# Kernel tuning notes

Measured on AMD Instinct MI355X. Metric: run time of the kernel, lower is better.

## Reference

```python
import jax, jax.numpy as jnp
import numpy as np

GN_GROUPS = 32
GN_EPS = 1e-5


def conv1x1(x, w, b):
    # x: [B,C,H,W], w: [O,C], b: [O]
    return jnp.einsum('bchw,oc->bohw', x, w) + b[None, :, None, None]


def maxpool2(x):
    B, C, H, W = x.shape
    return x.reshape(B, C, H // 2, 2, W // 2, 2).max(axis=(3, 5))


def group_norm(x, w, b, groups=GN_GROUPS, eps=GN_EPS):
    B, C, H, W = x.shape
    xg = x.reshape(B, groups, -1)
    m = xg.mean(axis=-1, keepdims=True)
    v = xg.var(axis=-1, keepdims=True)
    xn = ((xg - m) * jax.lax.rsqrt(v + eps)).reshape(B, C, H, W)
    return xn * w[None, :, None, None] + b[None, :, None, None]


def setup_inputs() -> dict:
    key = jax.random.key(0)
    ks = jax.random.split(key, 8)
    B, C, Ci, H, W = 4, 128, 64, 96, 96
    s_in = 1.0 / np.sqrt(C)
    s_ic = 1.0 / np.sqrt(Ci)
    return {
        'x': jax.random.normal(ks[0], (B, C, H, W), jnp.float32),
        'w_theta': jax.random.normal(ks[1], (Ci, C), jnp.float32) * s_in,
        'b_theta': jnp.zeros((Ci,), jnp.float32),
        'w_phi': jax.random.normal(ks[2], (Ci, C), jnp.float32) * s_in,
        'b_phi': jnp.zeros((Ci,), jnp.float32),
        'w_g': jax.random.normal(ks[3], (Ci, C), jnp.float32) * s_in,
        'b_g': jnp.zeros((Ci,), jnp.float32),
        'w_W': jax.random.normal(ks[4], (C, Ci), jnp.float32) * s_ic,
        'b_W': jnp.zeros((C,), jnp.float32),
        'gn_w': jnp.ones((C,), jnp.float32),
        'gn_b': jnp.zeros((C,), jnp.float32),
    }


def reference(x, w_theta, b_theta, w_phi, b_phi, w_g, b_g, w_W, b_W, gn_w, gn_b):
    B, C, H, W = x.shape
    Ci = w_theta.shape[0]
    # projections (1x1 convs); phi and g are 2x2 max-pooled (sub_sample=True)
    theta = conv1x1(x, w_theta, b_theta).reshape(B, Ci, H * W)          # [B,Ci,N]
    phi = maxpool2(conv1x1(x, w_phi, b_phi)).reshape(B, Ci, -1)         # [B,Ci,N']
    g = maxpool2(conv1x1(x, w_g, b_g)).reshape(B, Ci, -1)               # [B,Ci,N']
    # unscaled single-head attention
    f = jnp.einsum('bcn,bcm->bnm', theta, phi)                          # [B,N,N']
    f = jax.nn.softmax(f, axis=-1)
    y = jnp.einsum('bnm,bcm->bcn', f, g).reshape(B, Ci, H, W)           # [B,Ci,H,W]
    w_y = group_norm(conv1x1(y, w_W, b_W), gn_w, gn_b)
    return w_y + x
```

## Files before the change

### kernel.cpp

```cpp
#include <hip/hip_runtime.h>
#include <math.h>

#define B_ 4
#define C_ 128
#define CI_ 64
#define H_ 96
#define W_ 96
#define HW_ (H_*W_)
#define NP_ 2304
#define GROUPS_ 32
#define EPS_ 1e-5f
#define KVT_ 32
#define NT_ (NP_/KVT_)
#define NBLK_ 288

typedef _Float16 f16x8 __attribute__((ext_vector_type(8)));
typedef _Float16 f16x2 __attribute__((ext_vector_type(2)));
typedef __attribute__((ext_vector_type(4))) float f32x4;

__device__ inline f32x4 mfma16h(f16x8 a, f16x8 b, f32x4 c) {
    return __builtin_amdgcn_mfma_f32_16x16x32_f16(a, b, c, 0, 0, 0);
}
__device__ inline float h2f(unsigned short s) {
    return (float)__builtin_bit_cast(_Float16, s);
}
__device__ inline unsigned pk_f16(float a, float b) {
    return __builtin_bit_cast(unsigned, __builtin_amdgcn_cvt_pkrtz(a, b));
}
__device__ inline f16x8 pk8(float v0, float v1, float v2, float v3,
                            float v4, float v5, float v6, float v7) {
    uint4 u = { pk_f16(v0, v1), pk_f16(v2, v3), pk_f16(v4, v5), pk_f16(v6, v7) };
    return __builtin_bit_cast(f16x8, u);
}
__device__ inline void gload_lds16(const void* g, void* l) {
    __builtin_amdgcn_global_load_lds(
        (const __attribute__((address_space(1))) void*)reinterpret_cast<uintptr_t>(g),
        (__attribute__((address_space(3))) void*)(unsigned)reinterpret_cast<uintptr_t>(l),
        16, 0, 0);
}

__global__ __launch_bounds__(256) void wprep_kernel(
    const float* __restrict__ w_theta, const float* __restrict__ w_phi,
    const float* __restrict__ w_g,     const float* __restrict__ w_W,
    unsigned short* __restrict__ Whall)
{
    const int idx = blockIdx.x * 256 + threadIdx.x;
    float v;
    if      (idx <  8192) v = w_theta[idx];
    else if (idx < 16384) v = w_phi[idx - 8192];
    else if (idx < 24576) v = w_g[idx - 16384];
    else                  v = w_W[idx - 24576];
    Whall[idx] = __builtin_bit_cast(unsigned short, (_Float16)v);
}

__global__ __launch_bounds__(128) void proj_kernel(
    const float* __restrict__ x, const unsigned short* __restrict__ Whall,
    const float* __restrict__ b_theta, const float* __restrict__ b_phi,
    const float* __restrict__ b_g,
    unsigned short* __restrict__ Qo, unsigned short* __restrict__ phiF,
    unsigned short* __restrict__ gF)
{
    __shared__ __align__(16) unsigned short pb[2][16 * 72];

    const int t    = threadIdx.x;
    const int wv   = t >> 6;
    const int lane = t & 63;
    const int lr   = lane & 15;
    const int lg   = lane >> 4;
    const int b    = blockIdx.y;
    const int px0  = blockIdx.x * 32 + wv * 16;

    const float* xb = x + (size_t)b * C_ * HW_ + px0 + lr;
    f16x8 xa[4];
    #pragma unroll
    for (int u = 0; u < 4; ++u) {
        const float* p = xb + (size_t)(u * 32 + lg * 8) * HW_;
        xa[u] = pk8(p[0], p[(size_t)HW_], p[2 * (size_t)HW_], p[3 * (size_t)HW_],
                    p[4 * (size_t)HW_], p[5 * (size_t)HW_], p[6 * (size_t)HW_],
                    p[7 * (size_t)HW_]);
    }

    #pragma unroll
    for (int mat = 0; mat < 3; ++mat) {
        const unsigned short* Whp = Whall + mat * 8192;
        const float* bsel = (mat == 0) ? b_theta : (mat == 1) ? b_phi : b_g;
        unsigned short* osel = (mat == 0) ? Qo : (mat == 1) ? phiF : gF;

        f32x4 D[4];
        #pragma unroll
        for (int ct = 0; ct < 4; ++ct) D[ct] = (f32x4){0.f, 0.f, 0.f, 0.f};
        #pragma unroll
        for (int u = 0; u < 4; ++u)
            #pragma unroll
            for (int ct = 0; ct < 4; ++ct) {
                f16x8 wb = *(const f16x8*)&Whp[(ct * 16 + lr) * 128 + u * 32 + lg * 8];
                D[ct] = mfma16h(xa[u], wb, D[ct]);
            }

        #pragma unroll
        for (int ct = 0; ct < 4; ++ct) {
            const float bi = bsel[ct * 16 + lr];
            #pragma unroll
            for (int r2 = 0; r2 < 4; ++r2)
                pb[wv][(4 * lg + r2) * 72 + ct * 16 + lr] =
                    __builtin_bit_cast(unsigned short, (_Float16)(D[ct][r2] + bi));
        }
        {
            const int px = lane >> 2, ch = lane & 3;
            f16x8 y0 = *(const f16x8*)&pb[wv][px * 72 + ch * 16];
            f16x8 y1 = *(const f16x8*)&pb[wv][px * 72 + ch * 16 + 8];
            unsigned short* op = osel + ((size_t)b * HW_ + px0 + px) * CI_ + ch * 16;
            *(f16x8*)op       = y0;
            *(f16x8*)(op + 8) = y1;
        }
    }
}

__global__ __launch_bounds__(256) void pool_kernel(
    const unsigned short* __restrict__ phiF, const unsigned short* __restrict__ gF,
    unsigned short* __restrict__ Ko, unsigned short* __restrict__ Vt)
{
    __shared__ unsigned short vbuf[32][66];
    const int t  = threadIdx.x;
    const int b  = blockIdx.y;
    const int m0 = blockIdx.x * 32;

    {
        const int ci = t & 63;
        #pragma unroll
        for (int i = 0; i < 8; ++i) {
            const int ml = (t >> 6) + 4 * i;
            const int m  = m0 + ml;
            const int ph = m / 48, pw = m % 48;
            const size_t base = ((size_t)b * HW_ + (ph * 2) * W_ + pw * 2) * CI_ + ci;
            const unsigned short* pk_ = phiF + base;
            const unsigned short* pg_ = gF + base;
            float kv = fmaxf(fmaxf(h2f(pk_[0]), h2f(pk_[CI_])),
                             fmaxf(h2f(pk_[(size_t)W_ * CI_]), h2f(pk_[(size_t)(W_ + 1) * CI_])));
            float gv = fmaxf(fmaxf(h2f(pg_[0]), h2f(pg_[CI_])),
                             fmaxf(h2f(pg_[(size_t)W_ * CI_]), h2f(pg_[(size_t)(W_ + 1) * CI_])));
            Ko[((size_t)b * NP_ + m) * CI_ + ci] =
                __builtin_bit_cast(unsigned short, (_Float16)kv);
            vbuf[ml][ci] = __builtin_bit_cast(unsigned short, (_Float16)gv);
        }
    }
    __syncthreads();
    {
        const int ml = t & 31;
        const int ms = (8 * ((ml >> 2) & 3) + 4 * ((ml >> 4) & 1) + (ml & 3));
        #pragma unroll
        for (int i = 0; i < 8; ++i) {
            const int ci = (t >> 5) + 8 * i;
            Vt[((size_t)b * CI_ + ci) * NP_ + m0 + ms] = vbuf[ml][ci];
        }
    }
}

__global__ __launch_bounds__(128) void attn_kernel(
    const unsigned short* __restrict__ Qg, const unsigned short* __restrict__ Kg,
    const unsigned short* __restrict__ Vt, unsigned short* __restrict__ Yh)
{
    __shared__ unsigned char Klds[2][4096];
    __shared__ unsigned char Vlds[2][4096];

    const int t    = threadIdx.x;
    const int wv   = t >> 6;
    const int lane = t & 63;
    const int lr   = lane & 15;
    const int lg   = lane >> 4;
    const int b    = blockIdx.y;
    const int q0   = blockIdx.x * 32 + wv * 16;

    const int krow = lane >> 3;
    const int kchk = (lane & 7) ^ krow;
    const int vrow = lane >> 2;
    const int vchk = (lane & 3) ^ (vrow & 3);

    const unsigned short* Kb = Kg + (size_t)b * NP_ * CI_;
    const unsigned short* Vb = Vt + (size_t)b * CI_ * NP_;

    f16x8 qf[2];
    #pragma unroll
    for (int u = 0; u < 2; ++u)
        qf[u] = *(const f16x8*)(Qg + ((size_t)b * HW_ + q0 + lr) * CI_ + u * 32 + lg * 8);

    f32x4 o_acc[4];
    #pragma unroll
    for (int dt = 0; dt < 4; ++dt) o_acc[dt] = (f32x4){0.f, 0.f, 0.f, 0.f};
    float mrun = -1e30f, lrun = 0.f;

#define STAGE(BUF, TT)                                                          \
    {                                                                           \
        const int kv0_ = (TT) * KVT_;                                           \
        if (wv == 0) {                                                          \
            _Pragma("unroll")                                                   \
            for (int i = 0; i < 4; ++i)                                         \
                gload_lds16(Kb + (size_t)(kv0_ + 8 * i + krow) * CI_ + kchk * 8,\
                            &Klds[BUF][i * 1024]);                              \
        } else {                                                                \
            _Pragma("unroll")                                                   \
            for (int i = 0; i < 4; ++i)                                         \
                gload_lds16(Vb + (size_t)(16 * i + vrow) * NP_ + kv0_ + vchk * 8,\
                            &Vlds[BUF][i * 1024]);                              \
        }                                                                       \
    }

#define COMPUTE(BUF)                                                            \
    {                                                                           \
        f16x8 kf[2][2];                                                         \
        _Pragma("unroll")                                                       \
        for (int u = 0; u < 2; ++u)                                             \
            _Pragma("unroll")                                                   \
            for (int k4 = 0; k4 < 2; ++k4)                                      \
                kf[u][k4] = *(const f16x8*)&Klds[BUF][(k4 * 16 + lr) * 128      \
                                + (((4 * u + lg) ^ (lr & 7)) << 4)];            \
        f32x4 s[2];                                                             \
        s[0] = (f32x4){0.f, 0.f, 0.f, 0.f};                                     \
        s[1] = (f32x4){0.f, 0.f, 0.f, 0.f};                                     \
        __builtin_amdgcn_s_setprio(1);                                          \
        _Pragma("unroll")                                                       \
        for (int u = 0; u < 2; ++u) {                                           \
            s[0] = mfma16h(kf[u][0], qf[u], s[0]);                              \
            s[1] = mfma16h(kf[u][1], qf[u], s[1]);                              \
        }                                                                       \
        __builtin_amdgcn_s_setprio(0);                                          \
        float tmax = fmaxf(fmaxf(fmaxf(s[0][0], s[0][1]),                       \
                                 fmaxf(s[0][2], s[0][3])),                      \
                           fmaxf(fmaxf(s[1][0], s[1][1]),                       \
                                 fmaxf(s[1][2], s[1][3])));                     \
        if (!__all(tmax <= mrun + 8.0f)) {                                      \
            tmax = fmaxf(tmax, __shfl_xor(tmax, 16));                           \
            tmax = fmaxf(tmax, __shfl_xor(tmax, 32));                           \
            const float mnew = fmaxf(mrun, tmax);                               \
            const float sc = __expf(mrun - mnew);                               \
            lrun *= sc;                                                         \
            _Pragma("unroll")                                                   \
            for (int r2 = 0; r2 < 4; ++r2) {                                    \
                const float scb = __shfl(sc, 4 * lg + r2);                      \
                _Pragma("unroll")                                               \
                for (int dt = 0; dt < 4; ++dt) o_acc[dt][r2] *= scb;            \
            }                                                                   \
            mrun = mnew;                                                        \
        }                                                                       \
        const float e00 = __expf(s[0][0] - mrun);                               \
        const float e01 = __expf(s[0][1] - mrun);                               \
        const float e02 = __expf(s[0][2] - mrun);                               \
        const float e03 = __expf(s[0][3] - mrun);                               \
        const float e10 = __expf(s[1][0] - mrun);                               \
        const float e11 = __expf(s[1][1] - mrun);                               \
        const float e12 = __expf(s[1][2] - mrun);                               \
        const float e13 = __expf(s[1][3] - mrun);                               \
        lrun += ((e00 + e01) + (e02 + e03)) + ((e10 + e11) + (e12 + e13));      \
        f16x8 pf = pk8(e00, e01, e02, e03, e10, e11, e12, e13);                 \
        __builtin_amdgcn_s_setprio(1);                                          \
        _Pragma("unroll")                                                       \
        for (int dt = 0; dt < 4; ++dt) {                                        \
            const int vrow_ = dt * 16 + lr;                                     \
            f16x8 vf = *(const f16x8*)&Vlds[BUF][vrow_ * 64                     \
                            + (((lg ^ (lr & 3))) << 4)];                        \
            o_acc[dt] = mfma16h(pf, vf, o_acc[dt]);                             \
        }                                                                       \
        __builtin_amdgcn_s_setprio(0);                                          \
    }

    STAGE(0, 0);
    STAGE(1, 1);

    for (int it = 0; it < NT_ / 2; ++it) {
        const int t0 = 2 * it;
        asm volatile("s_waitcnt vmcnt(4)" ::: "memory");
        __builtin_amdgcn_s_barrier();
        COMPUTE(0);
        __builtin_amdgcn_s_barrier();
        if (t0 + 2 < NT_) STAGE(0, t0 + 2);
        if (it == NT_ / 2 - 1) {
            asm volatile("s_waitcnt vmcnt(0)" ::: "memory");
        } else {
            asm volatile("s_waitcnt vmcnt(4)" ::: "memory");
        }
        __builtin_amdgcn_s_barrier();
        COMPUTE(1);
        __builtin_amdgcn_s_barrier();
        if (t0 + 3 < NT_) STAGE(1, t0 + 3);
    }

    float lt = lrun;
    lt += __shfl_xor(lt, 16);
    lt += __shfl_xor(lt, 32);
    unsigned short* yb = (unsigned short*)&Klds[wv][0];
    #pragma unroll
    for (int r2 = 0; r2 < 4; ++r2) {
        const float inv = 1.0f / __shfl(lt, 4 * lg + r2);
        #pragma unroll
        for (int dt = 0; dt < 4; ++dt)
            yb[(4 * lg + r2) * 72 + dt * 16 + lr] =
                __builtin_bit_cast(unsigned short, (_Float16)(o_acc[dt][r2] * inv));
    }
    {
        const int px = lane >> 2, ch = lane & 3;
        f16x8 y0 = *(const f16x8*)&yb[px * 72 + ch * 16];
        f16x8 y1 = *(const f16x8*)&yb[px * 72 + ch * 16 + 8];
        unsigned short* op = Yh + ((size_t)b * HW_ + q0 + px) * CI_ + ch * 16;
        *(f16x8*)op       = y0;
        *(f16x8*)(op + 8) = y1;
    }
#undef STAGE
#undef COMPUTE
}

__global__ __launch_bounds__(128) void conv2_kernel(
    const unsigned short* __restrict__ Yh, const unsigned short* __restrict__ wWh,
    const float* __restrict__ bW, unsigned short* __restrict__ Zh,
    float* __restrict__ gpart)
{
    __shared__ float wpart[2][32][2];

    const int t    = threadIdx.x;
    const int wv   = t >> 6;
    const int lane = t & 63;
    const int lr   = lane & 15;
    const int lg   = lane >> 4;
    const int b    = blockIdx.y;
    const int n0   = blockIdx.x * 32 + wv * 16;

    f16x8 ya[2];
    #pragma unroll
    for (int u = 0; u < 2; ++u)
        ya[u] = *(const f16x8*)(Yh + ((size_t)b * HW_ + n0 + lr) * CI_ + u * 32 + lg * 8);

    unsigned short* Zb = Zh + (size_t)b * C_ * HW_ + n0 + lr;
    #pragma unroll
    for (int ot = 0; ot < 8; ++ot) {
        f32x4 D = (f32x4){0.f, 0.f, 0.f, 0.f};
        #pragma unroll
        for (int u = 0; u < 2; ++u) {
            f16x8 wa = *(const f16x8*)&wWh[(ot * 16 + lr) * CI_ + u * 32 + lg * 8];
            D = mfma16h(wa, ya[u], D);
        }
        float zs = 0.f, zq = 0.f;
        #pragma unroll
        for (int r2 = 0; r2 < 4; ++r2) {
            const int o = ot * 16 + 4 * lg + r2;
            const float z = D[r2] + bW[o];
            Zb[(size_t)o * HW_] = __builtin_bit_cast(unsigned short, (_Float16)z);
            zs += z;
            zq += z * z;
        }
        zs += __shfl_xor(zs, 1);  zq += __shfl_xor(zq, 1);
        zs += __shfl_xor(zs, 2);  zq += __shfl_xor(zq, 2);
        zs += __shfl_xor(zs, 4);  zq += __shfl_xor(zq, 4);
        zs += __shfl_xor(zs, 8);  zq += __shfl_xor(zq, 8);
        if (lr == 0) {
            wpart[wv][ot * 4 + lg][0] = zs;
            wpart[wv][ot * 4 + lg][1] = zq;
        }
    }
    __syncthreads();
    if (t < 64) {
        const int g = t >> 1, w = t & 1;
        const float v = wpart[0][g][w] + wpart[1][g][w];
        gpart[(((size_t)b * NBLK_ + blockIdx.x) * 32 + g) * 2 + w] = v;
    }
}

__global__ __launch_bounds__(256) void final_kernel(
    const unsigned short* __restrict__ Zh, const float* __restrict__ xg,
    const float* __restrict__ gpart, const float* __restrict__ gnw,
    const float* __restrict__ gnb, float* __restrict__ out)
{
    __shared__ float red[256][2];
    const int t = threadIdx.x;
    const int c = blockIdx.x;
    const int b = blockIdx.y;
    const int zc = blockIdx.z;
    const int g = c >> 2;

    float v1 = 0.f, v2 = 0.f;
    for (int j = t; j < NBLK_; j += 256) {
        v1 += gpart[(((size_t)b * NBLK_ + j) * 32 + g) * 2 + 0];
        v2 += gpart[(((size_t)b * NBLK_ + j) * 32 + g) * 2 + 1];
    }
    red[t][0] = v1; red[t][1] = v2;
    __syncthreads();
    for (int off = 128; off > 0; off >>= 1) {
        if (t < off) { red[t][0] += red[t + off][0]; red[t][1] += red[t + off][1]; }
        __syncthreads();
    }
    const float invn = 1.0f / (4 * HW_);
    const float mean = red[0][0] * invn;
    const float var  = red[0][1] * invn - mean * mean;
    const float rstd = rsqrtf(var + EPS_);
    const float sc = rstd * gnw[c];
    const float sh = gnb[c] - mean * sc;

    const unsigned short* zp = Zh + ((size_t)b * C_ + c) * HW_;
    const float4* xp = (const float4*)(xg + ((size_t)b * C_ + c) * HW_);
    float4*       op = (float4*)(out + ((size_t)b * C_ + c) * HW_);
    #pragma unroll
    for (int i = 0; i < 3; ++i) {
        const int j = (zc * 3 + i) * 256 + t;
        const ushort4 zv = *(const ushort4*)(zp + (size_t)j * 4);
        const float4 xv = xp[j];
        float4 o;
        o.x = h2f(zv.x) * sc + sh + xv.x;
        o.y = h2f(zv.y) * sc + sh + xv.y;
        o.z = h2f(zv.z) * sc + sh + xv.z;
        o.w = h2f(zv.w) * sc + sh + xv.w;
        op[j] = o;
    }
}

extern "C" void kernel_launch(void* const* d_in, const int* in_sizes, int n_in,
                              void* d_out, int out_size, void* d_ws, size_t ws_size,
                              hipStream_t stream)
{
    const float* x       = (const float*)d_in[0];
    const float* w_theta = (const float*)d_in[1];
    const float* b_theta = (const float*)d_in[2];
    const float* w_phi   = (const float*)d_in[3];
    const float* b_phi   = (const float*)d_in[4];
    const float* w_g     = (const float*)d_in[5];
    const float* b_g     = (const float*)d_in[6];
    const float* w_W     = (const float*)d_in[7];
    const float* b_W     = (const float*)d_in[8];
    const float* gn_w    = (const float*)d_in[9];
    const float* gn_b    = (const float*)d_in[10];
    float* out = (float*)d_out;
    char* wsb  = (char*)d_ws;

    unsigned short* Q    = (unsigned short*)(wsb);
    unsigned short* K    = (unsigned short*)(wsb +  4718592);
    unsigned short* Vt   = (unsigned short*)(wsb +  5898240);
    unsigned short* phiF = (unsigned short*)(wsb +  7077888);
    unsigned short* gF   = (unsigned short*)(wsb + 11796480);
    unsigned short* Yh   = (unsigned short*)(wsb +  7077888);
    float* gpart         = (float*)(wsb + 11796480);
    unsigned short* Zh   = (unsigned short*)(wsb + 16515072);
    unsigned short* Whall= (unsigned short*)(wsb + 35390464);
    unsigned short* wWh  = Whall + 24576;

    wprep_kernel<<<128, 256, 0, stream>>>(w_theta, w_phi, w_g, w_W, Whall);
    proj_kernel <<<dim3(NBLK_, B_), 128, 0, stream>>>(
        x, Whall, b_theta, b_phi, b_g, Q, phiF, gF);
    pool_kernel <<<dim3(NP_ / 32, B_), 256, 0, stream>>>(phiF, gF, K, Vt);
    attn_kernel <<<dim3(HW_ / 32, B_), 128, 0, stream>>>(Q, K, Vt, Yh);
    conv2_kernel<<<dim3(NBLK_, B_), 128, 0, stream>>>(Yh, wWh, b_W, Zh, gpart);
    final_kernel<<<dim3(C_, B_, 3), 256, 0, stream>>>(Zh, x, gpart, gn_w, gn_b, out);
}
```

Measured before the change: 104.3 us.

## Fuse 2x2 max-pool of phi and g into projection kernel

The projection kernel now tiles pixels as 2-row by 16-column patches so each block holds complete 2x2 pooling windows. It max-pools phi and g in LDS and writes pooled K and transposed V directly, which removes the full-resolution phiF/gF intermediates and the separate pool kernel launch. In exchange it adds block-wide barriers inside the projection loop and narrower, scattered Vt stores.

```diff
diff --git a/kernel.cpp b/kernel.cpp
--- a/kernel.cpp
+++ b/kernel.cpp
@@ -32,6 +32,12 @@
     uint4 u = { pk_f16(v0, v1), pk_f16(v2, v3), pk_f16(v4, v5), pk_f16(v6, v7) };
     return __builtin_bit_cast(f16x8, u);
 }
+__device__ inline unsigned short hmax4(unsigned short a, unsigned short b,
+                                       unsigned short c, unsigned short d) {
+    unsigned short m = (h2f(a) >= h2f(b)) ? a : b;
+    unsigned short n = (h2f(c) >= h2f(d)) ? c : d;
+    return (h2f(m) >= h2f(n)) ? m : n;
+}
 __device__ inline void gload_lds16(const void* g, void* l) {
     __builtin_amdgcn_global_load_lds(
         (const __attribute__((address_space(1))) void*)reinterpret_cast<uintptr_t>(g),
@@ -57,8 +63,8 @@
     const float* __restrict__ x, const unsigned short* __restrict__ Whall,
     const float* __restrict__ b_theta, const float* __restrict__ b_phi,
     const float* __restrict__ b_g,
-    unsigned short* __restrict__ Qo, unsigned short* __restrict__ phiF,
-    unsigned short* __restrict__ gF)
+    unsigned short* __restrict__ Qo, unsigned short* __restrict__ Ko,
+    unsigned short* __restrict__ Vt)
 {
     __shared__ __align__(16) unsigned short pb[2][16 * 72];
 
@@ -68,9 +74,12 @@
     const int lr   = lane & 15;
     const int lg   = lane >> 4;
     const int b    = blockIdx.y;
-    const int px0  = blockIdx.x * 32 + wv * 16;
-
-    const float* xb = x + (size_t)b * C_ * HW_ + px0 + lr;
+    const int h0   = (blockIdx.x / 6) * 2;
+    const int w0   = (blockIdx.x % 6) * 16;
+    const int nb   = (h0 + wv) * W_ + w0;
+    const int m0   = (h0 >> 1) * 48 + (w0 >> 1);
+
+    const float* xb = x + (size_t)b * C_ * HW_ + nb + lr;
     f16x8 xa[4];
     #pragma unroll
     for (int u = 0; u < 4; ++u) {
@@ -84,7 +93,6 @@
     for (int mat = 0; mat < 3; ++mat) {
         const unsigned short* Whp = Whall + mat * 8192;
         const float* bsel = (mat == 0) ? b_theta : (mat == 1) ? b_phi : b_g;
-        unsigned short* osel = (mat == 0) ? Qo : (mat == 1) ? phiF : gF;
 
         f32x4 D[4];
         #pragma unroll
@@ -105,53 +113,41 @@
                 pb[wv][(4 * lg + r2) * 72 + ct * 16 + lr] =
                     __builtin_bit_cast(unsigned short, (_Float16)(D[ct][r2] + bi));
         }
-        {
+
+        if (mat == 0) {
             const int px = lane >> 2, ch = lane & 3;
             f16x8 y0 = *(const f16x8*)&pb[wv][px * 72 + ch * 16];
             f16x8 y1 = *(const f16x8*)&pb[wv][px * 72 + ch * 16 + 8];
-            unsigned short* op = osel + ((size_t)b * HW_ + px0 + px) * CI_ + ch * 16;
+            unsigned short* op = Qo + ((size_t)b * HW_ + nb + px) * CI_ + ch * 16;
             *(f16x8*)op       = y0;
             *(f16x8*)(op + 8) = y1;
-        }
-    }
-}
-
-__global__ __launch_bounds__(256) void pool_kernel(
-    const unsigned short* __restrict__ phiF, const unsigned short* __restrict__ gF,
-    unsigned short* __restrict__ Ko, unsigned short* __restrict__ Vt)
-{
-    __shared__ unsigned short vbuf[32][66];
-    const int t  = threadIdx.x;
-    const int b  = blockIdx.y;
-    const int m0 = blockIdx.x * 32;
-
-    {
-        const int ci = t & 63;
-        #pragma unroll
-        for (int i = 0; i < 8; ++i) {
-            const int ml = (t >> 6) + 4 * i;
-            const int m  = m0 + ml;
-            const int ph = m / 48, pw = m % 48;
-            const size_t base = ((size_t)b * HW_ + (ph * 2) * W_ + pw * 2) * CI_ + ci;
-            const unsigned short* pk_ = phiF + base;
-            const unsigned short* pg_ = gF + base;
-            float kv = fmaxf(fmaxf(h2f(pk_[0]), h2f(pk_[CI_])),
-                             fmaxf(h2f(pk_[(size_t)W_ * CI_]), h2f(pk_[(size_t)(W_ + 1) * CI_])));
-            float gv = fmaxf(fmaxf(h2f(pg_[0]), h2f(pg_[CI_])),
-                             fmaxf(h2f(pg_[(size_t)W_ * CI_]), h2f(pg_[(size_t)(W_ + 1) * CI_])));
-            Ko[((size_t)b * NP_ + m) * CI_ + ci] =
-                __builtin_bit_cast(unsigned short, (_Float16)kv);
-            vbuf[ml][ci] = __builtin_bit_cast(unsigned short, (_Float16)gv);
-        }
-    }
-    __syncthreads();
-    {
-        const int ml = t & 31;
-        const int ms = (8 * ((ml >> 2) & 3) + 4 * ((ml >> 4) & 1) + (ml & 3));
-        #pragma unroll
-        for (int i = 0; i < 8; ++i) {
-            const int ci = (t >> 5) + 8 * i;
-            Vt[((size_t)b * CI_ + ci) * NP_ + m0 + ms] = vbuf[ml][ci];
+        } else if (mat == 1) {
+            __syncthreads();
+            const int w = t >> 4, ci0 = (t & 15) * 4;
+            unsigned short r[4];
+            #pragma unroll
+            for (int j = 0; j < 4; ++j) {
+                const int ci = ci0 + j;
+                r[j] = hmax4(pb[0][(2 * w) * 72 + ci], pb[0][(2 * w + 1) * 72 + ci],
+                             pb[1][(2 * w) * 72 + ci], pb[1][(2 * w + 1) * 72 + ci]);
+            }
+            *(ushort4*)&Ko[((size_t)b * NP_ + m0 + w) * CI_ + ci0] =
+                (ushort4){r[0], r[1], r[2], r[3]};
+            __syncthreads();
+        } else {
+            __syncthreads();
+            const int ci = t >> 1, pr = t & 1;
+            #pragma unroll
+            for (int j = 0; j < 4; ++j) {
+                const int w = pr * 4 + j;
+                unsigned short v = hmax4(
+                    pb[0][(2 * w) * 72 + ci], pb[0][(2 * w + 1) * 72 + ci],
+                    pb[1][(2 * w) * 72 + ci], pb[1][(2 * w + 1) * 72 + ci]);
+                const int m  = m0 + w;
+                const int ms = (m & ~31)
+                             | (8 * ((m >> 2) & 3) + 4 * ((m >> 4) & 1) + (m & 3));
+                Vt[((size_t)b * CI_ + ci) * NP_ + ms] = v;
+            }
         }
     }
 }
@@ -431,8 +427,6 @@
     unsigned short* Q    = (unsigned short*)(wsb);
     unsigned short* K    = (unsigned short*)(wsb +  4718592);
     unsigned short* Vt   = (unsigned short*)(wsb +  5898240);
-    unsigned short* phiF = (unsigned short*)(wsb +  7077888);
-    unsigned short* gF   = (unsigned short*)(wsb + 11796480);
     unsigned short* Yh   = (unsigned short*)(wsb +  7077888);
     float* gpart         = (float*)(wsb + 11796480);
     unsigned short* Zh   = (unsigned short*)(wsb + 16515072);
@@ -440,9 +434,8 @@
     unsigned short* wWh  = Whall + 24576;
 
     wprep_kernel<<<128, 256, 0, stream>>>(w_theta, w_phi, w_g, w_W, Whall);
-    proj_kernel <<<dim3(NBLK_, B_), 128, 0, stream>>>(
-        x, Whall, b_theta, b_phi, b_g, Q, phiF, gF);
-    pool_kernel <<<dim3(NP_ / 32, B_), 256, 0, stream>>>(phiF, gF, K, Vt);
+    proj_kernel <<<dim3(288, B_), 128, 0, stream>>>(
+        x, Whall, b_theta, b_phi, b_g, Q, K, Vt);
     attn_kernel <<<dim3(HW_ / 32, B_), 128, 0, stream>>>(Q, K, Vt, Yh);
     conv2_kernel<<<dim3(NBLK_, B_), 128, 0, stream>>>(Yh, wWh, b_W, Zh, gpart);
     final_kernel<<<dim3(C_, B_, 3), 256, 0, stream>>>(Zh, x, gpart, gn_w, gn_b, out);
```

Result: faster. 101.7 us (-2.4%).
